# Performance work log

Measured on AMD Instinct MI355X. Metric: run time of the kernel, lower is better.

The kernel has to match this reference:

```python
import jax, jax.numpy as jnp
import numpy as np

EPS = 1e-12  # torch F.normalize eps


def _pairwise_unit_diffs(x):
    # x: [B, N, D] -> unit-normalized pairwise diffs [B, N*N, D]
    B, N, D = x.shape
    d = x[:, :, None, :] - x[:, None, :, :]            # [B, N, N, D]
    n = jnp.linalg.norm(d, axis=-1, keepdims=True)
    d = d / jnp.maximum(n, EPS)                        # zero rows stay zero
    return d.reshape(B, N * N, D)


def setup_inputs() -> dict:
    key = jax.random.key(0)
    k1, k2 = jax.random.split(key)
    B, N, D = 4, 64, 128
    student = jax.random.normal(k1, (B, N, D), dtype=jnp.float32)
    teacher = jax.random.normal(k2, (B, N, D), dtype=jnp.float32)
    return {"student": student, "teacher": teacher}


def reference(student, teacher):
    B, N, D = student.shape
    sd = _pairwise_unit_diffs(student)                              # [B, N^2, D]
    td = jax.lax.stop_gradient(_pairwise_unit_diffs(teacher))      # [B, N^2, D]
    s_ang = jnp.einsum('bkd,bld->bkl', sd, sd)
    t_ang = jax.lax.stop_gradient(jnp.einsum('bkd,bld->bkl', td, td))
    # smooth L1 (beta=1.0), summed then divided by total element count
    diff = s_ang - t_ang
    ad = jnp.abs(diff)
    loss = jnp.where(ad < 1.0, 0.5 * diff * diff, ad - 0.5)
    count = B * (N * N) * (N * N)
    return jnp.sum(loss) / count
```

## Files before the change

kernel.cpp:

```cpp
#include <hip/hip_runtime.h>


#define EPSF 1e-12f

__device__ __forceinline__ float rinv_from_nsq(float nsq)
{
    float n = sqrtf(fmaxf(nsq, 0.0f));
    return 1.0f / fmaxf(n, EPSF);
}

__global__ __launch_bounds__(512) void fused_kernel(
    const float* __restrict__ student, const float* __restrict__ teacher,
    float* __restrict__ out)
{
    __shared__ float Gs[4096];
    __shared__ float Gt[4096];
    __shared__ float pool[4352];
    __shared__ float red[8];

    int b   = blockIdx.x / 63;
    int kc  = blockIdx.x % 63;
    int tid = threadIdx.x;

    const float* Xsg = student + b * 8192;
    const float* Xtg = teacher + b * 8192;

    int which = tid >> 8;
    int pos8  = tid & 255;
    int pgA   = pos8 & 15;
    int qgA   = pos8 >> 4;
    const float* XldsC = pool + which * 2176;

    float c[4][4];
#pragma unroll
    for (int i = 0; i < 4; ++i)
#pragma unroll
        for (int j = 0; j < 4; ++j) c[i][j] = 0.f;

    int r   = tid >> 3;
    int f4i = tid & 7;

    for (int pc = 0; pc < 4; ++pc) {
        float4 a4 = *(const float4*)(Xsg + r * 128 + pc * 32 + f4i * 4);
        float4 b4 = *(const float4*)(Xtg + r * 128 + pc * 32 + f4i * 4);
        int d0 = f4i * 4;
        pool[(d0 + 0) * 68 + r] = a4.x;
        pool[(d0 + 1) * 68 + r] = a4.y;
        pool[(d0 + 2) * 68 + r] = a4.z;
        pool[(d0 + 3) * 68 + r] = a4.w;
        pool[2176 + (d0 + 0) * 68 + r] = b4.x;
        pool[2176 + (d0 + 1) * 68 + r] = b4.y;
        pool[2176 + (d0 + 2) * 68 + r] = b4.z;
        pool[2176 + (d0 + 3) * 68 + r] = b4.w;
        __syncthreads();

#pragma unroll 8
        for (int d = 0; d < 32; ++d) {
            float4 xp = *(const float4*)(XldsC + d * 68 + 4 * pgA);
            float4 xq = *(const float4*)(XldsC + d * 68 + 4 * qgA);
            c[0][0] = fmaf(xp.x, xq.x, c[0][0]);
            c[0][1] = fmaf(xp.x, xq.y, c[0][1]);
            c[0][2] = fmaf(xp.x, xq.z, c[0][2]);
            c[0][3] = fmaf(xp.x, xq.w, c[0][3]);
            c[1][0] = fmaf(xp.y, xq.x, c[1][0]);
            c[1][1] = fmaf(xp.y, xq.y, c[1][1]);
            c[1][2] = fmaf(xp.y, xq.z, c[1][2]);
            c[1][3] = fmaf(xp.y, xq.w, c[1][3]);
            c[2][0] = fmaf(xp.z, xq.x, c[2][0]);
            c[2][1] = fmaf(xp.z, xq.y, c[2][1]);
            c[2][2] = fmaf(xp.z, xq.z, c[2][2]);
            c[2][3] = fmaf(xp.z, xq.w, c[2][3]);
            c[3][0] = fmaf(xp.w, xq.x, c[3][0]);
            c[3][1] = fmaf(xp.w, xq.y, c[3][1]);
            c[3][2] = fmaf(xp.w, xq.z, c[3][2]);
            c[3][3] = fmaf(xp.w, xq.w, c[3][3]);
        }
        __syncthreads();
    }

    {
        float* Gd = which ? Gt : Gs;
#pragma unroll
        for (int i = 0; i < 4; ++i)
            *(float4*)&Gd[(4 * pgA + i) * 64 + 4 * qgA] =
                make_float4(c[i][0], c[i][1], c[i][2], c[i][3]);
    }
    __syncthreads();

    float* vs = pool;
    float* vt = pool + 2176;

    {
        int m  = tid >> 4;
        int q4 = (tid & 15) * 4;
        int t  = kc * 32 + m;
        int i = 0, rem = t;
        while (rem >= 63 - i) { rem -= 63 - i; ++i; }
        int j = i + 1 + rem;

        float rsij = rinv_from_nsq(Gs[i * 65] - 2.f * Gs[i * 64 + j] + Gs[j * 65]);
        float rtij = rinv_from_nsq(Gt[i * 65] - 2.f * Gt[i * 64 + j] + Gt[j * 65]);

        float4 gis = *(const float4*)(Gs + i * 64 + q4);
        float4 gjs = *(const float4*)(Gs + j * 64 + q4);
        float4 git = *(const float4*)(Gt + i * 64 + q4);
        float4 gjt = *(const float4*)(Gt + j * 64 + q4);
        float4 v;
        v.x = (gis.x - gjs.x) * rsij;
        v.y = (gis.y - gjs.y) * rsij;
        v.z = (gis.z - gjs.z) * rsij;
        v.w = (gis.w - gjs.w) * rsij;
        *(float4*)(vs + m * 68 + q4) = v;
        v.x = (git.x - gjt.x) * rtij;
        v.y = (git.y - gjt.y) * rtij;
        v.z = (git.z - gjt.z) * rtij;
        v.w = (git.w - gjt.w) * rtij;
        *(float4*)(vt + m * 68 + q4) = v;
    }

    int msub = tid >> 7;
    int pos  = tid & 127;
    int pg = 0, qg = 0;
    float4 rsv[4], rtv[4];
    if (pos < 120) {
        int rem = pos;
        while (rem >= 15 - pg) { rem -= 15 - pg; ++pg; }
        qg = pg + 1 + rem;
        int p4  = pg * 4;
        float dps[4], dpt[4];
#pragma unroll
        for (int cc = 0; cc < 4; ++cc) {
            dps[cc] = Gs[(p4 + cc) * 65];
            dpt[cc] = Gt[(p4 + cc) * 65];
        }
#pragma unroll
        for (int k = 0; k < 4; ++k) {
            int q = qg * 4 + k;
            float4 g = *(const float4*)(Gs + q * 64 + p4);
            float gqq = Gs[q * 65];
            rsv[k].x = rinv_from_nsq(dps[0] - 2.f * g.x + gqq);
            rsv[k].y = rinv_from_nsq(dps[1] - 2.f * g.y + gqq);
            rsv[k].z = rinv_from_nsq(dps[2] - 2.f * g.z + gqq);
            rsv[k].w = rinv_from_nsq(dps[3] - 2.f * g.w + gqq);
            float4 h = *(const float4*)(Gt + q * 64 + p4);
            float hqq = Gt[q * 65];
            rtv[k].x = rinv_from_nsq(dpt[0] - 2.f * h.x + hqq);
            rtv[k].y = rinv_from_nsq(dpt[1] - 2.f * h.y + hqq);
            rtv[k].z = rinv_from_nsq(dpt[2] - 2.f * h.z + hqq);
            rtv[k].w = rinv_from_nsq(dpt[3] - 2.f * h.w + hqq);
        }
    }
    __syncthreads();

    float ac0 = 0.f, ac1 = 0.f, ac2 = 0.f, ac3 = 0.f;

#define SL1(acc, spc, sqc, tpc, tqc, rsk, rtk)                                  \
    {                                                                           \
        float d  = (spc - sqc) * rsk - (tpc - tqc) * rtk;                       \
        float a  = fabsf(d);                                                    \
        float mn = fminf(a, 1.0f);                                              \
        acc = fmaf(mn, fmaf(-0.5f, mn, a), acc);                                \
    }

    if (pos < 120) {
        int p4  = pg * 4;
        int q4l = qg * 4;
#pragma unroll 4
        for (int mm = 0; mm < 8; ++mm) {
            int m = mm * 4 + msub;
            const float* vsm = vs + m * 68;
            const float* vtm = vt + m * 68;
            float4 sp = *(const float4*)(vsm + p4);
            float4 tp = *(const float4*)(vtm + p4);
            float4 sq = *(const float4*)(vsm + q4l);
            float4 tq = *(const float4*)(vtm + q4l);

            SL1(ac0, sp.x, sq.x, tp.x, tq.x, rsv[0].x, rtv[0].x)
            SL1(ac0, sp.y, sq.x, tp.y, tq.x, rsv[0].y, rtv[0].y)
            SL1(ac0, sp.z, sq.x, tp.z, tq.x, rsv[0].z, rtv[0].z)
            SL1(ac0, sp.w, sq.x, tp.w, tq.x, rsv[0].w, rtv[0].w)

            SL1(ac1, sp.x, sq.y, tp.x, tq.y, rsv[1].x, rtv[1].x)
            SL1(ac1, sp.y, sq.y, tp.y, tq.y, rsv[1].y, rtv[1].y)
            SL1(ac1, sp.z, sq.y, tp.z, tq.y, rsv[1].z, rtv[1].z)
            SL1(ac1, sp.w, sq.y, tp.w, tq.y, rsv[1].w, rtv[1].w)

            SL1(ac2, sp.x, sq.z, tp.x, tq.z, rsv[2].x, rtv[2].x)
            SL1(ac2, sp.y, sq.z, tp.y, tq.z, rsv[2].y, rtv[2].y)
            SL1(ac2, sp.z, sq.z, tp.z, tq.z, rsv[2].z, rtv[2].z)
            SL1(ac2, sp.w, sq.z, tp.w, tq.z, rsv[2].w, rtv[2].w)

            SL1(ac3, sp.x, sq.w, tp.x, tq.w, rsv[3].x, rtv[3].x)
            SL1(ac3, sp.y, sq.w, tp.y, tq.w, rsv[3].y, rtv[3].y)
            SL1(ac3, sp.z, sq.w, tp.z, tq.w, rsv[3].z, rtv[3].z)
            SL1(ac3, sp.w, sq.w, tp.w, tq.w, rsv[3].w, rtv[3].w)
        }
    }

    {
        int m  = tid >> 4;
        int g4 = (tid & 15) * 4;
        float4 s4 = *(const float4*)(vs + m * 68 + g4);
        float4 t4 = *(const float4*)(vt + m * 68 + g4);

        float d0s = Gs[(g4 + 0) * 65], d1s = Gs[(g4 + 1) * 65];
        float d2s = Gs[(g4 + 2) * 65], d3s = Gs[(g4 + 3) * 65];
        float d0t = Gt[(g4 + 0) * 65], d1t = Gt[(g4 + 1) * 65];
        float d2t = Gt[(g4 + 2) * 65], d3t = Gt[(g4 + 3) * 65];

        float rs01 = rinv_from_nsq(d0s - 2.f * Gs[(g4 + 0) * 64 + g4 + 1] + d1s);
        float rs02 = rinv_from_nsq(d0s - 2.f * Gs[(g4 + 0) * 64 + g4 + 2] + d2s);
        float rs03 = rinv_from_nsq(d0s - 2.f * Gs[(g4 + 0) * 64 + g4 + 3] + d3s);
        float rs12 = rinv_from_nsq(d1s - 2.f * Gs[(g4 + 1) * 64 + g4 + 2] + d2s);
        float rs13 = rinv_from_nsq(d1s - 2.f * Gs[(g4 + 1) * 64 + g4 + 3] + d3s);
        float rs23 = rinv_from_nsq(d2s - 2.f * Gs[(g4 + 2) * 64 + g4 + 3] + d3s);
        float rt01 = rinv_from_nsq(d0t - 2.f * Gt[(g4 + 0) * 64 + g4 + 1] + d1t);
        float rt02 = rinv_from_nsq(d0t - 2.f * Gt[(g4 + 0) * 64 + g4 + 2] + d2t);
        float rt03 = rinv_from_nsq(d0t - 2.f * Gt[(g4 + 0) * 64 + g4 + 3] + d3t);
        float rt12 = rinv_from_nsq(d1t - 2.f * Gt[(g4 + 1) * 64 + g4 + 2] + d2t);
        float rt13 = rinv_from_nsq(d1t - 2.f * Gt[(g4 + 1) * 64 + g4 + 3] + d3t);
        float rt23 = rinv_from_nsq(d2t - 2.f * Gt[(g4 + 2) * 64 + g4 + 3] + d3t);

        SL1(ac0, s4.x, s4.y, t4.x, t4.y, rs01, rt01)
        SL1(ac1, s4.x, s4.z, t4.x, t4.z, rs02, rt02)
        SL1(ac2, s4.x, s4.w, t4.x, t4.w, rs03, rt03)
        SL1(ac3, s4.y, s4.z, t4.y, t4.z, rs12, rt12)
        SL1(ac0, s4.y, s4.w, t4.y, t4.w, rs13, rt13)
        SL1(ac1, s4.z, s4.w, t4.z, t4.w, rs23, rt23)
    }
#undef SL1

    float acc = (ac0 + ac1) + (ac2 + ac3);

    for (int off = 32; off > 0; off >>= 1)
        acc += __shfl_down(acc, off);
    int lane = tid & 63;
    int wave = tid >> 6;
    if (lane == 0) red[wave] = acc;
    __syncthreads();
    if (tid < 8) {
        float v = red[tid];
        v += __shfl_down(v, 4);
        v += __shfl_down(v, 2);
        v += __shfl_down(v, 1);
        if (tid == 0) atomicAdd(out, v * (1.0f / 16777216.0f));
    }
}

extern "C" void kernel_launch(void* const* d_in, const int* in_sizes, int n_in,
                              void* d_out, int out_size, void* d_ws, size_t ws_size,
                              hipStream_t stream)
{
    const float* student = (const float*)d_in[0];
    const float* teacher = (const float*)d_in[1];
    (void)d_ws; (void)ws_size;
    fused_kernel<<<252, 512, 0, stream>>>(student, teacher, (float*)d_out);
}
```

Measured before the change: 75.41 us.

## Compute only upper-triangle Gram tiles with split-K and mirror via transpose

```diff
diff --git a/kernel.cpp b/kernel.cpp
--- a/kernel.cpp
+++ b/kernel.cpp
@@ -15,49 +15,59 @@
 {
     __shared__ float Gs[4096];
     __shared__ float Gt[4096];
-    __shared__ float pool[4352];
+    __shared__ float Xp_lds[17408];
     __shared__ float red[8];
 
     int b   = blockIdx.x / 63;
     int kc  = blockIdx.x % 63;
     int tid = threadIdx.x;
 
-    const float* Xsg = student + b * 8192;
-    const float* Xtg = teacher + b * 8192;
-
-    int which = tid >> 8;
-    int pos8  = tid & 255;
-    int pgA   = pos8 & 15;
-    int qgA   = pos8 >> 4;
-    const float* XldsC = pool + which * 2176;
-
+    {
+        int r  = tid >> 3;
+        int f8 = tid & 7;
+        const float* Xs_row = student + b * 8192 + r * 128;
+        const float* Xt_row = teacher + b * 8192 + r * 128;
+#pragma unroll
+        for (int k = 0; k < 4; ++k) {
+            int d4 = f8 * 4 + k;
+            float4 a  = *(const float4*)(Xs_row + d4 * 4);
+            float4 bb = *(const float4*)(Xt_row + d4 * 4);
+            int dbase = d4 * 4;
+            Xp_lds[(dbase + 0) * 68 + r] = a.x;
+            Xp_lds[(dbase + 1) * 68 + r] = a.y;
+            Xp_lds[(dbase + 2) * 68 + r] = a.z;
+            Xp_lds[(dbase + 3) * 68 + r] = a.w;
+            Xp_lds[8704 + (dbase + 0) * 68 + r] = bb.x;
+            Xp_lds[8704 + (dbase + 1) * 68 + r] = bb.y;
+            Xp_lds[8704 + (dbase + 2) * 68 + r] = bb.z;
+            Xp_lds[8704 + (dbase + 3) * 68 + r] = bb.w;
+        }
+    }
+    __syncthreads();
+
+    bool is_strict = tid < 480;
+    int h = 0, whA = 0, pgA = 0, qgA = 0;
     float c[4][4];
 #pragma unroll
     for (int i = 0; i < 4; ++i)
 #pragma unroll
         for (int j = 0; j < 4; ++j) c[i][j] = 0.f;
 
-    int r   = tid >> 3;
-    int f4i = tid & 7;
-
-    for (int pc = 0; pc < 4; ++pc) {
-        float4 a4 = *(const float4*)(Xsg + r * 128 + pc * 32 + f4i * 4);
-        float4 b4 = *(const float4*)(Xtg + r * 128 + pc * 32 + f4i * 4);
-        int d0 = f4i * 4;
-        pool[(d0 + 0) * 68 + r] = a4.x;
-        pool[(d0 + 1) * 68 + r] = a4.y;
-        pool[(d0 + 2) * 68 + r] = a4.z;
-        pool[(d0 + 3) * 68 + r] = a4.w;
-        pool[2176 + (d0 + 0) * 68 + r] = b4.x;
-        pool[2176 + (d0 + 1) * 68 + r] = b4.y;
-        pool[2176 + (d0 + 2) * 68 + r] = b4.z;
-        pool[2176 + (d0 + 3) * 68 + r] = b4.w;
-        __syncthreads();
-
+    if (is_strict) {
+        h = tid & 1;
+        int t2 = tid >> 1;
+        whA = t2 / 120;
+        int t = t2 % 120;
+        int rem = t;
+        while (rem >= 15 - pgA) { rem -= 15 - pgA; ++pgA; }
+        qgA = pgA + 1 + rem;
+
+        const float* Xb = Xp_lds + whA * 8704;
+        int d0 = h * 64;
 #pragma unroll 8
-        for (int d = 0; d < 32; ++d) {
-            float4 xp = *(const float4*)(XldsC + d * 68 + 4 * pgA);
-            float4 xq = *(const float4*)(XldsC + d * 68 + 4 * qgA);
+        for (int d = d0; d < d0 + 64; ++d) {
+            float4 xp = *(const float4*)(Xb + d * 68 + 4 * pgA);
+            float4 xq = *(const float4*)(Xb + d * 68 + 4 * qgA);
             c[0][0] = fmaf(xp.x, xq.x, c[0][0]);
             c[0][1] = fmaf(xp.x, xq.y, c[0][1]);
             c[0][2] = fmaf(xp.x, xq.z, c[0][2]);
@@ -75,20 +85,92 @@
             c[3][2] = fmaf(xp.w, xq.z, c[3][2]);
             c[3][3] = fmaf(xp.w, xq.w, c[3][3]);
         }
-        __syncthreads();
-    }
-
+        if (h == 0) {
+            float* Gd = whA ? Gt : Gs;
+#pragma unroll
+            for (int i = 0; i < 4; ++i)
+                *(float4*)&Gd[(4 * pgA + i) * 64 + 4 * qgA] =
+                    make_float4(c[i][0], c[i][1], c[i][2], c[i][3]);
+        }
+    } else {
+        int td = tid - 480;
+        int w2 = td >> 4;
+        int g  = td & 15;
+        float* Gd = w2 ? Gt : Gs;
+        float4 z = make_float4(0.f, 0.f, 0.f, 0.f);
+#pragma unroll
+        for (int i = 0; i < 4; ++i)
+            *(float4*)&Gd[(4 * g + i) * 64 + 4 * g] = z;
+    }
+    __syncthreads();
+
+    if (is_strict && h == 1) {
+        float* Gd = whA ? Gt : Gs;
+#pragma unroll
+        for (int i = 0; i < 4; ++i)
+#pragma unroll
+            for (int j = 0; j < 4; ++j)
+                atomicAdd(&Gd[(4 * pgA + i) * 64 + 4 * qgA + j], c[i][j]);
+    }
     {
-        float* Gd = which ? Gt : Gs;
+        int w2    = tid >> 8;
+        int dtile = (tid >> 4) & 15;
+        int dd0   = (tid & 15) * 8;
+        const float* Xb = Xp_lds + w2 * 8704;
+        float cd[4][4];
 #pragma unroll
         for (int i = 0; i < 4; ++i)
-            *(float4*)&Gd[(4 * pgA + i) * 64 + 4 * qgA] =
-                make_float4(c[i][0], c[i][1], c[i][2], c[i][3]);
-    }
-    __syncthreads();
-
-    float* vs = pool;
-    float* vt = pool + 2176;
+#pragma unroll
+            for (int j = 0; j < 4; ++j) cd[i][j] = 0.f;
+#pragma unroll
+        for (int d = dd0; d < dd0 + 8; ++d) {
+            float4 x = *(const float4*)(Xb + d * 68 + 4 * dtile);
+            cd[0][0] = fmaf(x.x, x.x, cd[0][0]);
+            cd[0][1] = fmaf(x.x, x.y, cd[0][1]);
+            cd[0][2] = fmaf(x.x, x.z, cd[0][2]);
+            cd[0][3] = fmaf(x.x, x.w, cd[0][3]);
+            cd[1][0] = fmaf(x.y, x.x, cd[1][0]);
+            cd[1][1] = fmaf(x.y, x.y, cd[1][1]);
+            cd[1][2] = fmaf(x.y, x.z, cd[1][2]);
+            cd[1][3] = fmaf(x.y, x.w, cd[1][3]);
+            cd[2][0] = fmaf(x.z, x.x, cd[2][0]);
+            cd[2][1] = fmaf(x.z, x.y, cd[2][1]);
+            cd[2][2] = fmaf(x.z, x.z, cd[2][2]);
+            cd[2][3] = fmaf(x.z, x.w, cd[2][3]);
+            cd[3][0] = fmaf(x.w, x.x, cd[3][0]);
+            cd[3][1] = fmaf(x.w, x.y, cd[3][1]);
+            cd[3][2] = fmaf(x.w, x.z, cd[3][2]);
+            cd[3][3] = fmaf(x.w, x.w, cd[3][3]);
+        }
+        float* Gd = w2 ? Gt : Gs;
+#pragma unroll
+        for (int i = 0; i < 4; ++i)
+#pragma unroll
+            for (int j = 0; j < 4; ++j)
+                atomicAdd(&Gd[(4 * dtile + i) * 64 + 4 * dtile + j], cd[i][j]);
+    }
+    __syncthreads();
+
+    if (tid < 240) {
+        int w2 = tid / 120;
+        int t  = tid % 120;
+        int pg = 0, rem = t;
+        while (rem >= 15 - pg) { rem -= 15 - pg; ++pg; }
+        int qg = pg + 1 + rem;
+        float* Gd = w2 ? Gt : Gs;
+#pragma unroll
+        for (int i = 0; i < 4; ++i) {
+            float4 v = *(const float4*)&Gd[(4 * pg + i) * 64 + 4 * qg];
+            Gd[(4 * qg + 0) * 64 + 4 * pg + i] = v.x;
+            Gd[(4 * qg + 1) * 64 + 4 * pg + i] = v.y;
+            Gd[(4 * qg + 2) * 64 + 4 * pg + i] = v.z;
+            Gd[(4 * qg + 3) * 64 + 4 * pg + i] = v.w;
+        }
+    }
+    __syncthreads();
+
+    float* vs = Xp_lds;
+    float* vt = Xp_lds + 2176;
 
     {
         int m  = tid >> 4;
@@ -142,12 +224,12 @@
             rsv[k].y = rinv_from_nsq(dps[1] - 2.f * g.y + gqq);
             rsv[k].z = rinv_from_nsq(dps[2] - 2.f * g.z + gqq);
             rsv[k].w = rinv_from_nsq(dps[3] - 2.f * g.w + gqq);
-            float4 h = *(const float4*)(Gt + q * 64 + p4);
+            float4 hh = *(const float4*)(Gt + q * 64 + p4);
             float hqq = Gt[q * 65];
-            rtv[k].x = rinv_from_nsq(dpt[0] - 2.f * h.x + hqq);
-            rtv[k].y = rinv_from_nsq(dpt[1] - 2.f * h.y + hqq);
-            rtv[k].z = rinv_from_nsq(dpt[2] - 2.f * h.z + hqq);
-            rtv[k].w = rinv_from_nsq(dpt[3] - 2.f * h.w + hqq);
+            rtv[k].x = rinv_from_nsq(dpt[0] - 2.f * hh.x + hqq);
+            rtv[k].y = rinv_from_nsq(dpt[1] - 2.f * hh.y + hqq);
+            rtv[k].z = rinv_from_nsq(dpt[2] - 2.f * hh.z + hqq);
+            rtv[k].w = rinv_from_nsq(dpt[3] - 2.f * hh.w + hqq);
         }
     }
     __syncthreads();
```

After: 92.28 us. 1.22x slower.

## Compute per-batch Gram matrices with split-bf16 MFMA instead of scalar FMA

Applied to the files above, without the earlier changes.

```diff
diff --git a/kernel.cpp b/kernel.cpp
--- a/kernel.cpp
+++ b/kernel.cpp
@@ -2,11 +2,25 @@
 
 
 #define EPSF 1e-12f
+
+typedef __bf16 bf16x8 __attribute__((ext_vector_type(8)));
+typedef float  f32x4  __attribute__((ext_vector_type(4)));
 
 __device__ __forceinline__ float rinv_from_nsq(float nsq)
 {
     float n = sqrtf(fmaxf(nsq, 0.0f));
     return 1.0f / fmaxf(n, EPSF);
+}
+
+__device__ __forceinline__ void cvt8(float4 u, float4 v, bf16x8& h, bf16x8& l)
+{
+    float uu[8] = {u.x, u.y, u.z, u.w, v.x, v.y, v.z, v.w};
+#pragma unroll
+    for (int i = 0; i < 8; ++i) {
+        __bf16 hh = (__bf16)uu[i];
+        h[i] = hh;
+        l[i] = (__bf16)(uu[i] - (float)hh);
+    }
 }
 
 __global__ __launch_bounds__(512) void fused_kernel(
@@ -15,75 +29,74 @@
 {
     __shared__ float Gs[4096];
     __shared__ float Gt[4096];
-    __shared__ float pool[4352];
+    __shared__ __align__(16) float pool[17408];
     __shared__ float red[8];
 
     int b   = blockIdx.x / 63;
     int kc  = blockIdx.x % 63;
     int tid = threadIdx.x;
 
-    const float* Xsg = student + b * 8192;
-    const float* Xtg = teacher + b * 8192;
-
-    int which = tid >> 8;
-    int pos8  = tid & 255;
-    int pgA   = pos8 & 15;
-    int qgA   = pos8 >> 4;
-    const float* XldsC = pool + which * 2176;
-
-    float c[4][4];
-#pragma unroll
-    for (int i = 0; i < 4; ++i)
-#pragma unroll
-        for (int j = 0; j < 4; ++j) c[i][j] = 0.f;
-
-    int r   = tid >> 3;
-    int f4i = tid & 7;
-
-    for (int pc = 0; pc < 4; ++pc) {
-        float4 a4 = *(const float4*)(Xsg + r * 128 + pc * 32 + f4i * 4);
-        float4 b4 = *(const float4*)(Xtg + r * 128 + pc * 32 + f4i * 4);
-        int d0 = f4i * 4;
-        pool[(d0 + 0) * 68 + r] = a4.x;
-        pool[(d0 + 1) * 68 + r] = a4.y;
-        pool[(d0 + 2) * 68 + r] = a4.z;
-        pool[(d0 + 3) * 68 + r] = a4.w;
-        pool[2176 + (d0 + 0) * 68 + r] = b4.x;
-        pool[2176 + (d0 + 1) * 68 + r] = b4.y;
-        pool[2176 + (d0 + 2) * 68 + r] = b4.z;
-        pool[2176 + (d0 + 3) * 68 + r] = b4.w;
-        __syncthreads();
-
-#pragma unroll 8
-        for (int d = 0; d < 32; ++d) {
-            float4 xp = *(const float4*)(XldsC + d * 68 + 4 * pgA);
-            float4 xq = *(const float4*)(XldsC + d * 68 + 4 * qgA);
-            c[0][0] = fmaf(xp.x, xq.x, c[0][0]);
-            c[0][1] = fmaf(xp.x, xq.y, c[0][1]);
-            c[0][2] = fmaf(xp.x, xq.z, c[0][2]);
-            c[0][3] = fmaf(xp.x, xq.w, c[0][3]);
-            c[1][0] = fmaf(xp.y, xq.x, c[1][0]);
-            c[1][1] = fmaf(xp.y, xq.y, c[1][1]);
-            c[1][2] = fmaf(xp.y, xq.z, c[1][2]);
-            c[1][3] = fmaf(xp.y, xq.w, c[1][3]);
-            c[2][0] = fmaf(xp.z, xq.x, c[2][0]);
-            c[2][1] = fmaf(xp.z, xq.y, c[2][1]);
-            c[2][2] = fmaf(xp.z, xq.z, c[2][2]);
-            c[2][3] = fmaf(xp.z, xq.w, c[2][3]);
-            c[3][0] = fmaf(xp.w, xq.x, c[3][0]);
-            c[3][1] = fmaf(xp.w, xq.y, c[3][1]);
-            c[3][2] = fmaf(xp.w, xq.z, c[3][2]);
-            c[3][3] = fmaf(xp.w, xq.w, c[3][3]);
-        }
-        __syncthreads();
-    }
-
-    {
-        float* Gd = which ? Gt : Gs;
-#pragma unroll
-        for (int i = 0; i < 4; ++i)
-            *(float4*)&Gd[(4 * pgA + i) * 64 + 4 * qgA] =
-                make_float4(c[i][0], c[i][1], c[i][2], c[i][3]);
+    {
+        int r  = tid >> 3;
+        int f8 = tid & 7;
+        const float* Xs = student + b * 8192 + r * 128 + f8 * 16;
+        const float* Xt = teacher + b * 8192 + r * 128 + f8 * 16;
+        float* sHi = pool + 0 * 4352 + r * 68 + f8 * 8;
+        float* sLo = pool + 1 * 4352 + r * 68 + f8 * 8;
+        float* tHi = pool + 2 * 4352 + r * 68 + f8 * 8;
+        float* tLo = pool + 3 * 4352 + r * 68 + f8 * 8;
+#pragma unroll
+        for (int c = 0; c < 2; ++c) {
+            float4 u = *(const float4*)(Xs + c * 8);
+            float4 v = *(const float4*)(Xs + c * 8 + 4);
+            bf16x8 h, l;
+            cvt8(u, v, h, l);
+            *(bf16x8*)(sHi + c * 4) = h;
+            *(bf16x8*)(sLo + c * 4) = l;
+            u = *(const float4*)(Xt + c * 8);
+            v = *(const float4*)(Xt + c * 8 + 4);
+            cvt8(u, v, h, l);
+            *(bf16x8*)(tHi + c * 4) = h;
+            *(bf16x8*)(tLo + c * 4) = l;
+        }
+    }
+    __syncthreads();
+
+    {
+        int wid  = tid >> 6;
+        int lane = tid & 63;
+        int l15  = lane & 15;
+        int quad = lane >> 4;
+        int tensor = wid >> 2;
+        int mt     = wid & 3;
+        const float* XH = pool + tensor * 8704;
+        const float* XL = XH + 4352;
+
+        bf16x8 aH[4], aL[4];
+        int abase = (mt * 16 + l15) * 68 + quad * 4;
+#pragma unroll
+        for (int ks = 0; ks < 4; ++ks) {
+            aH[ks] = *(const bf16x8*)(XH + abase + ks * 16);
+            aL[ks] = *(const bf16x8*)(XL + abase + ks * 16);
+        }
+        float* Gd = tensor ? Gt : Gs;
+#pragma unroll
+        for (int nt = 0; nt < 4; ++nt) {
+            f32x4 acc = {0.f, 0.f, 0.f, 0.f};
+            int bbase = (nt * 16 + l15) * 68 + quad * 4;
+#pragma unroll
+            for (int ks = 0; ks < 4; ++ks) {
+                bf16x8 bH = *(const bf16x8*)(XH + bbase + ks * 16);
+                bf16x8 bL = *(const bf16x8*)(XL + bbase + ks * 16);
+                acc = __builtin_amdgcn_mfma_f32_16x16x32_bf16(aH[ks], bH, acc, 0, 0, 0);
+                acc = __builtin_amdgcn_mfma_f32_16x16x32_bf16(aH[ks], bL, acc, 0, 0, 0);
+                acc = __builtin_amdgcn_mfma_f32_16x16x32_bf16(aL[ks], bH, acc, 0, 0, 0);
+                acc = __builtin_amdgcn_mfma_f32_16x16x32_bf16(aL[ks], bL, acc, 0, 0, 0);
+            }
+#pragma unroll
+            for (int reg = 0; reg < 4; ++reg)
+                Gd[(mt * 16 + quad * 4 + reg) * 64 + nt * 16 + l15] = acc[reg];
+        }
     }
     __syncthreads();
 
@@ -142,12 +155,12 @@
             rsv[k].y = rinv_from_nsq(dps[1] - 2.f * g.y + gqq);
             rsv[k].z = rinv_from_nsq(dps[2] - 2.f * g.z + gqq);
             rsv[k].w = rinv_from_nsq(dps[3] - 2.f * g.w + gqq);
-            float4 h = *(const float4*)(Gt + q * 64 + p4);
+            float4 hh = *(const float4*)(Gt + q * 64 + p4);
             float hqq = Gt[q * 65];
-            rtv[k].x = rinv_from_nsq(dpt[0] - 2.f * h.x + hqq);
-            rtv[k].y = rinv_from_nsq(dpt[1] - 2.f * h.y + hqq);
-            rtv[k].z = rinv_from_nsq(dpt[2] - 2.f * h.z + hqq);
-            rtv[k].w = rinv_from_nsq(dpt[3] - 2.f * h.w + hqq);
+            rtv[k].x = rinv_from_nsq(dpt[0] - 2.f * hh.x + hqq);
+            rtv[k].y = rinv_from_nsq(dpt[1] - 2.f * hh.y + hqq);
+            rtv[k].z = rinv_from_nsq(dpt[2] - 2.f * hh.z + hqq);
+            rtv[k].w = rinv_from_nsq(dpt[3] - 2.f * hh.w + hqq);
         }
     }
     __syncthreads();
```

After: 70.42 us. 1.07x faster.
